# Optimization experiments

Measured on AMD Instinct MI355X. Metric: run time of the kernel, lower is better.

Reference implementation:

```python
import math
import jax, jax.numpy as jnp
import numpy as np

N, M = 2048, 128            # fine grid points, coarse points
IN_NF, H, LMAX = 256, 128, 2
A2B = 1.88973
MIN_STD = 0.32 * A2B / 2.0  # two stddevs reach min covalent radius (Bohr)
MAX_STD = 2.32 * A2B / 2.0


def _sph_lmax2(d):
    # norm-normalized real spherical harmonics (e3nn convention), unit input d[..., 3]
    x, y, z = d[..., 0], d[..., 1], d[..., 2]
    s3 = math.sqrt(3.0)
    sh0 = jnp.ones_like(x)[..., None]                                    # [., 1]
    sh1 = jnp.stack([x, y, z], axis=-1)                                  # [., 3]
    sh2 = jnp.stack([s3 * x * z, s3 * x * y,
                     y * y - 0.5 * (x * x + z * z),
                     s3 * y * z, 0.5 * s3 * (z * z - x * x)], axis=-1)   # [., 5]
    return [sh0, sh1, sh2]


def _radial(dist, nb):
    # Gaussian radial basis; two stddevs span [MIN_COV_RAD, MAX_COV_RAD]
    s = jnp.linspace(MIN_STD, MAX_STD, nb, dtype=dist.dtype)
    temps = 2.0 * s * s
    x2 = dist[..., None] ** 2
    return jnp.exp(-x2 / temps) * (2.0 / 3.0) * x2 / temps / (math.pi * temps) ** 1.5


def setup_inputs():
    key = jax.random.key(0)
    k = jax.random.split(key, 10)
    xav = math.sqrt(6.0 / (H + H))
    return {
        'h': jax.random.normal(k[0], (N, IN_NF), jnp.float32),
        'grid_coords': jax.random.normal(k[1], (N, 3), jnp.float32),
        'coarse_coords': jax.random.normal(k[2], (M, 3), jnp.float32),
        'grid_weights': jax.random.uniform(k[3], (N,), jnp.float32),
        'W_pre': jax.random.normal(k[4], (IN_NF, H), jnp.float32) * math.sqrt(2.0 / (IN_NF + H)),
        'b_pre': jnp.zeros((H,), jnp.float32),
        'W_down': jax.random.uniform(k[5], (LMAX + 1, H, H), jnp.float32, -xav, xav),
        'W_up': jax.random.uniform(k[6], (LMAX + 1, H, H), jnp.float32, -xav, xav),
        'W_post': jax.random.normal(k[7], (H, H), jnp.float32) * math.sqrt(2.0 / (H + H)),
        'b_post': jnp.zeros((H,), jnp.float32),
    }


def reference(h, grid_coords, coarse_coords, grid_weights,
              W_pre, b_pre, W_down, W_up, W_post, b_post):
    h = jax.nn.silu(h @ W_pre + b_pre)                            # [N, H]
    # all-pairs directions/distances (vect_cdist); radius_cutoff = inf -> every pair is an edge
    dvec = grid_coords[:, None, :] - coarse_coords[None, :, :]    # [N, M, 3]
    dist = jnp.sqrt((dvec * dvec + 1e-20).sum(-1))                # [N, M]
    dirs = dvec / dist[..., None]
    sh = _sph_lmax2(dirs)                                         # list of [N, M, 2l+1]
    rad = _radial(dist, H)                                        # [N, M, H]
    # tp_down: paths (0e x le -> le); l=0 uses the scalar branch (no 1/sqrt(2l+1))
    # radial gating per hidden channel + quadrature integration onto coarse nodes
    coarse = []
    for l in range(LMAX + 1):
        norm = 1.0 if l == 0 else math.sqrt(2 * l + 1)
        c = jnp.einsum('nu,uw,nmj,nmw,n->mwj',
                       h, W_down[l], sh[l], rad, grid_weights) / norm
        coarse.append(c)                                          # [M, H, 2l+1]
    # tp_up: paths (le x le -> 0e); l>0 branch divides by sqrt(2l+1); scatter back to grid
    out = 0.0
    for l in range(LMAX + 1):
        norm = 1.0 if l == 0 else math.sqrt(2 * l + 1)
        out = out + jnp.einsum('mui,uw,nmi->nw', coarse[l], W_up[l], sh[l]) / norm
    return jax.nn.silu(out @ W_post + b_post)                     # [N, H]
```

## Files before the change

kernel.cpp:

```cpp
#include <hip/hip_runtime.h>
#include <math.h>

#define N_PTS 2048
#define M_PTS 128
#define INNF  256
#define H     128

#define MIN_STDC 0.30235680f
#define MAX_STDC 2.19208680f
#define PI_F     3.14159265358979f
#define LOG2E_F  1.44269504089f

static __device__ __forceinline__ float silu_f(float x) {
  return x / (1.0f + __expf(-x));
}

__global__ __launch_bounds__(256) void k_pre(const float* __restrict__ h,
    const float* __restrict__ W_pre, const float* __restrict__ b_pre,
    const float* __restrict__ W_down, const float* __restrict__ gw,
    float* __restrict__ hdg4) {
  __shared__ float h_lds[4 * INNF];
  __shared__ float hp_lds[4 * H];
  __shared__ float red[4 * 3 * H];
  int t = threadIdx.x;
  int n0 = blockIdx.x * 4;
  int lw  = t & 31;
  int row = (t >> 5) & 3;
  int uh  = t >> 7;
  int w0 = lw * 4;
  int n  = n0 + row;

  {
    int r4 = t >> 6, c4i = (t & 63) << 2;
    *(float4*)&h_lds[r4 * INNF + c4i] =
        *(const float4*)(h + (size_t)(n0 + r4) * INNF + c4i);
  }
  __syncthreads();

  float a1[4] = {};
  for (int u = uh * 128; u < uh * 128 + 128; u += 2) {
    float hv0 = h_lds[row * INNF + u];
    float hv1 = h_lds[row * INNF + u + 1];
    float4 wv0 = *(const float4*)(W_pre + (size_t)u * H + w0);
    float4 wv1 = *(const float4*)(W_pre + (size_t)(u + 1) * H + w0);
    a1[0] += hv0 * wv0.x + hv1 * wv1.x;
    a1[1] += hv0 * wv0.y + hv1 * wv1.y;
    a1[2] += hv0 * wv0.z + hv1 * wv1.z;
    a1[3] += hv0 * wv0.w + hv1 * wv1.w;
  }
  if (uh == 1) {
    #pragma unroll
    for (int i = 0; i < 4; ++i) red[row * H + w0 + i] = a1[i];
  }
  __syncthreads();
  if (uh == 0) {
    float4 bv = *(const float4*)(b_pre + w0);
    float bb[4] = {bv.x, bv.y, bv.z, bv.w};
    #pragma unroll
    for (int i = 0; i < 4; ++i)
      hp_lds[row * H + w0 + i] = silu_f(a1[i] + red[row * H + w0 + i] + bb[i]);
  }
  __syncthreads();

  float a2[3][4] = {};
  for (int u = uh * 64; u < uh * 64 + 64; ++u) {
    float p = hp_lds[row * H + u];
    #pragma unroll
    for (int l = 0; l < 3; ++l) {
      float4 wv = *(const float4*)(W_down + ((size_t)l * H + u) * H + w0);
      a2[l][0] += p * wv.x; a2[l][1] += p * wv.y;
      a2[l][2] += p * wv.z; a2[l][3] += p * wv.w;
    }
  }
  if (uh == 1) {
    #pragma unroll
    for (int l = 0; l < 3; ++l)
      #pragma unroll
      for (int i = 0; i < 4; ++i)
        red[(row * 3 + l) * H + w0 + i] = a2[l][i];
  }
  __syncthreads();
  if (uh == 0) {
    const float stp = (MAX_STDC - MIN_STDC) / 127.0f;
    const float invn1 = 0.57735026919f, invn2 = 0.44721359550f;
    float gwv = gw[n];
    #pragma unroll
    for (int i = 0; i < 4; ++i) {
      int w = w0 + i;
      float s = MIN_STDC + (float)w * stp;
      float temps = 2.0f * s * s;
      float coef = (2.0f / 3.0f) / (temps * powf(PI_F * temps, 1.5f));
      float sc = gwv * coef;
      float v0 = (a2[0][i] + red[(row * 3 + 0) * H + w]) * sc;
      float v1 = (a2[1][i] + red[(row * 3 + 1) * H + w]) * sc * invn1;
      float v2 = (a2[2][i] + red[(row * 3 + 2) * H + w]) * sc * invn2;
      *(float4*)(hdg4 + ((size_t)n * H + w) * 4) = make_float4(v0, v1, v2, 0.0f);
    }
  }
}

__global__ __launch_bounds__(256) void k_down(const float* __restrict__ gc,
    const float* __restrict__ cc, const float* __restrict__ hdg4,
    float* __restrict__ c_part) {
  __shared__ float lds[4608];
  int t = threadIdx.x;
  int m0 = blockIdx.x * 4;
  int ss = blockIdx.y;
  int n0 = ss * 64;
  int w  = t & 127;
  int nh = t >> 7;

  {
    int n_loc = t >> 2, m_loc = t & 3;
    int n = n0 + n_loc, m = m0 + m_loc;
    float dx = gc[3*n]   - cc[3*m];
    float dy = gc[3*n+1] - cc[3*m+1];
    float dz = gc[3*n+2] - cc[3*m+2];
    float d2 = dx*dx + dy*dy + dz*dz + 3e-20f;
    float inv = rsqrtf(d2);
    float x = dx*inv, y = dy*inv, z = dz*inv;
    const float s3 = 1.73205080757f;
    float* dst = &lds[(size_t)t * 12];
    dst[0] = 1.0f; dst[1] = x; dst[2] = y; dst[3] = z;
    dst[4] = s3*x*z; dst[5] = s3*x*y; dst[6] = y*y - 0.5f*(x*x + z*z);
    dst[7] = s3*y*z; dst[8] = 0.5f*s3*(z*z - x*x);
    dst[9] = d2; dst[10] = 0.0f; dst[11] = 0.0f;
  }
  __syncthreads();

  const float stp = (MAX_STDC - MIN_STDC) / 127.0f;
  float sw = MIN_STDC + (float)w * stp;
  float m_nl2t = -LOG2E_F / (2.0f * sw * sw);

  float acc[4][9] = {};
  for (int j = 0; j < 32; j += 4) {
    float4 hv[4];
    #pragma unroll
    for (int q = 0; q < 4; ++q)
      hv[q] = *(const float4*)(hdg4 + ((size_t)(n0 + nh*32 + j + q)*H + w)*4);
    #pragma unroll
    for (int q = 0; q < 4; ++q) {
      const float* shb = &lds[(size_t)(nh*32 + j + q) * 48];
      #pragma unroll
      for (int mm = 0; mm < 4; ++mm) {
        float4 q0 = *(const float4*)(shb + mm*12);
        float4 q1 = *(const float4*)(shb + mm*12 + 4);
        float4 q2 = *(const float4*)(shb + mm*12 + 8);
        float e  = exp2f(q2.y * m_nl2t);
        float rp = e * q2.y;
        float t0 = hv[q].x*rp, t1 = hv[q].y*rp, t2 = hv[q].z*rp;
        acc[mm][0] += t0;
        acc[mm][1] += t1*q0.y; acc[mm][2] += t1*q0.z; acc[mm][3] += t1*q0.w;
        acc[mm][4] += t2*q1.x; acc[mm][5] += t2*q1.y;
        acc[mm][6] += t2*q1.z; acc[mm][7] += t2*q1.w;
        acc[mm][8] += t2*q2.x;
      }
    }
  }

  __syncthreads();
  if (nh == 1) {
    #pragma unroll
    for (int mm = 0; mm < 4; ++mm)
      #pragma unroll
      for (int li = 0; li < 9; ++li)
        lds[(mm*9 + li)*128 + w] = acc[mm][li];
  }
  __syncthreads();
  if (nh == 0) {
    #pragma unroll
    for (int mm = 0; mm < 4; ++mm)
      #pragma unroll
      for (int li = 0; li < 9; ++li) {
        float v = acc[mm][li] + lds[(mm*9 + li)*128 + w];
        c_part[(((size_t)ss*M_PTS + m0 + mm)*9 + li)*H + w] = v;
      }
  }
}

__global__ __launch_bounds__(128) void k_cu(const float* __restrict__ c_part,
    const float* __restrict__ W_up, float* __restrict__ CU9) {
  __shared__ float c_lds[H];
  int t = threadIdx.x;
  int m = blockIdx.x, li = blockIdx.y;
  float v = 0.0f;
  #pragma unroll 8
  for (int s = 0; s < 32; ++s)
    v += c_part[(((size_t)s*M_PTS + m)*9 + li)*H + t];
  c_lds[t] = v;
  __syncthreads();

  int l = (li == 0) ? 0 : (li < 4 ? 1 : 2);
  const float invn[3] = {1.0f, 0.57735026919f, 0.44721359550f};
  float acc = 0.0f;
  for (int u = 0; u < H; u += 4) {
    float w0 = W_up[((size_t)l*H + u + 0)*H + t];
    float w1 = W_up[((size_t)l*H + u + 1)*H + t];
    float w2 = W_up[((size_t)l*H + u + 2)*H + t];
    float w3 = W_up[((size_t)l*H + u + 3)*H + t];
    acc += c_lds[u]*w0 + c_lds[u+1]*w1 + c_lds[u+2]*w2 + c_lds[u+3]*w3;
  }
  CU9[((size_t)m*9 + li)*H + t] = acc * invn[l];
}

__global__ __launch_bounds__(256) void k_up(const float* __restrict__ gc,
    const float* __restrict__ cc, const float* __restrict__ CU9,
    float* __restrict__ out_part) {
  __shared__ float At[72 * 36];
  __shared__ float Bl[72 * 128];
  int t = threadIdx.x;
  int n0 = blockIdx.x * 32;
  int ks = blockIdx.y;
  int wq  = t & 31;
  int tgn = t >> 5;
  int w0 = wq * 4;

  {
    int ch = t >> 7, idx = t & 127;
    int n_loc = idx >> 2, m_loc = idx & 3;
    int mrel = ch*4 + m_loc;
    int n = n0 + n_loc, m = ks*8 + mrel;
    float dx = gc[3*n]   - cc[3*m];
    float dy = gc[3*n+1] - cc[3*m+1];
    float dz = gc[3*n+2] - cc[3*m+2];
    float d2 = dx*dx + dy*dy + dz*dz + 3e-20f;
    float inv = rsqrtf(d2);
    float x = dx*inv, y = dy*inv, z = dz*inv;
    const float s3 = 1.73205080757f;
    float sh[9];
    sh[0] = 1.0f; sh[1] = x; sh[2] = y; sh[3] = z;
    sh[4] = s3*x*z; sh[5] = s3*x*y; sh[6] = y*y - 0.5f*(x*x + z*z);
    sh[7] = s3*y*z; sh[8] = 0.5f*s3*(z*z - x*x);
    #pragma unroll
    for (int li = 0; li < 9; ++li)
      At[(mrel*9 + li)*36 + n_loc] = sh[li];
  }
  #pragma unroll
  for (int i = 0; i < 9; ++i) {
    int idx = t + i*256;
    *(float4*)&Bl[idx*4] = *(const float4*)(CU9 + (size_t)ks*72*H + idx*4);
  }
  __syncthreads();

  float acc[4][4] = {};
  #pragma unroll 8
  for (int k = 0; k < 72; ++k) {
    float4 a = *(const float4*)&At[k*36 + 4*tgn];
    float4 b = *(const float4*)&Bl[k*128 + w0];
    float av[4] = {a.x, a.y, a.z, a.w};
    float bv[4] = {b.x, b.y, b.z, b.w};
    #pragma unroll
    for (int r = 0; r < 4; ++r)
      #pragma unroll
      for (int c = 0; c < 4; ++c)
        acc[r][c] += av[r] * bv[c];
  }
  #pragma unroll
  for (int r = 0; r < 4; ++r) {
    size_t row = (size_t)ks*N_PTS + n0 + 4*tgn + r;
    *(float4*)(out_part + row*H + w0) =
        make_float4(acc[r][0], acc[r][1], acc[r][2], acc[r][3]);
  }
}

__global__ __launch_bounds__(256) void k_post(const float* __restrict__ out_part,
    const float* __restrict__ W_post, const float* __restrict__ b_post,
    float* __restrict__ out) {
  __shared__ float op[4 * H];
  int t = threadIdx.x;
  int n0 = blockIdx.x * 4;
  int w = t & 127, nh = t >> 7;

  #pragma unroll
  for (int i = 0; i < 2; ++i) {
    int idx = t + i*256;
    int nl = idx >> 7, ww = idx & 127;
    float v = 0.0f;
    #pragma unroll
    for (int s = 0; s < 16; ++s)
      v += out_part[((size_t)s*N_PTS + n0 + nl)*H + ww];
    op[nl*H + ww] = v;
  }
  __syncthreads();

  float acc[2] = {0.0f, 0.0f};
  for (int u = 0; u < H; u += 4) {
    float4 p0 = *(const float4*)&op[(nh*2 + 0)*H + u];
    float4 p1 = *(const float4*)&op[(nh*2 + 1)*H + u];
    float w0 = W_post[(u+0)*H + w];
    float w1 = W_post[(u+1)*H + w];
    float w2 = W_post[(u+2)*H + w];
    float w3 = W_post[(u+3)*H + w];
    acc[0] += p0.x*w0 + p0.y*w1 + p0.z*w2 + p0.w*w3;
    acc[1] += p1.x*w0 + p1.y*w1 + p1.z*w2 + p1.w*w3;
  }
  float bp = b_post[w];
  out[(size_t)(n0 + nh*2 + 0)*H + w] = silu_f(acc[0] + bp);
  out[(size_t)(n0 + nh*2 + 1)*H + w] = silu_f(acc[1] + bp);
}

extern "C" void kernel_launch(void* const* d_in, const int* in_sizes, int n_in,
                              void* d_out, int out_size, void* d_ws, size_t ws_size,
                              hipStream_t stream) {
  const float* h      = (const float*)d_in[0];
  const float* gc     = (const float*)d_in[1];
  const float* cc     = (const float*)d_in[2];
  const float* gw     = (const float*)d_in[3];
  const float* W_pre  = (const float*)d_in[4];
  const float* b_pre  = (const float*)d_in[5];
  const float* W_down = (const float*)d_in[6];
  const float* W_up   = (const float*)d_in[7];
  const float* W_post = (const float*)d_in[8];
  const float* b_post = (const float*)d_in[9];

  float* ws       = (float*)d_ws;
  float* hdg4     = ws;
  float* c_part   = hdg4 + 1048576;
  float* CU9      = c_part + 4718592;
  float* out_part = c_part;
  float* out      = (float*)d_out;

  k_pre <<<512,           256, 0, stream>>>(h, W_pre, b_pre, W_down, gw, hdg4);
  k_down<<<dim3(32,32),   256, 0, stream>>>(gc, cc, hdg4, c_part);
  k_cu  <<<dim3(128,9),   128, 0, stream>>>(c_part, W_up, CU9);
  k_up  <<<dim3(64,16),   256, 0, stream>>>(gc, cc, CU9, out_part);
  k_post<<<512,           256, 0, stream>>>(out_part, W_post, b_post, out);
}
```

Before: 155.7 us.

## Stage W_pre and W_down tiles in LDS and process 8 rows per block

The pre-projection kernel now handles 8 grid points per block, with each of the 8 warps owning one row. Chunks of W_pre and W_down are cooperatively staged into shared memory and reused across all 8 rows. The old split-K across two half-blocks, with its shared-memory reduction, is removed, and the grid is halved. This targets redundant global weight reads at the cost of more synchronisation and a larger LDS footprint (about 60KB), which may limit occupancy. Only the first of five kernels changes, so the effect on total time is bounded.

```diff
diff --git a/kernel.cpp b/kernel.cpp
--- a/kernel.cpp
+++ b/kernel.cpp
@@ -19,70 +19,84 @@
     const float* __restrict__ W_pre, const float* __restrict__ b_pre,
     const float* __restrict__ W_down, const float* __restrict__ gw,
     float* __restrict__ hdg4) {
-  __shared__ float h_lds[4 * INNF];
-  __shared__ float hp_lds[4 * H];
-  __shared__ float red[4 * 3 * H];
-  int t = threadIdx.x;
-  int n0 = blockIdx.x * 4;
-  int lw  = t & 31;
-  int row = (t >> 5) & 3;
-  int uh  = t >> 7;
+  __shared__ float bigW[12288];
+  __shared__ float h_t[8 * INNF];
+  __shared__ float hp_t[8 * H];
+  int t = threadIdx.x;
+  int n0 = blockIdx.x * 8;
+  int lw = t & 31;
+  int g  = t >> 5;
   int w0 = lw * 4;
-  int n  = n0 + row;
-
+
+  #pragma unroll
+  for (int i = 0; i < 2; ++i) {
+    int idx = t + i * 256;
+    int row = idx >> 6, col = (idx & 63) << 2;
+    *(float4*)&h_t[row * INNF + col] =
+        *(const float4*)(h + (size_t)(n0 + row) * INNF + col);
+  }
+
+  float acc[4] = {};
+  for (int kc = 0; kc < 256; kc += 64) {
+    __syncthreads();
+    #pragma unroll
+    for (int i = 0; i < 8; ++i) {
+      int idx = t + i * 256;
+      *(float4*)&bigW[idx * 4] = *(const float4*)(W_pre + (size_t)kc * H + idx * 4);
+    }
+    __syncthreads();
+    #pragma unroll 4
+    for (int u4 = 0; u4 < 16; ++u4) {
+      float4 hv = *(const float4*)&h_t[g * INNF + kc + u4 * 4];
+      float hvv[4] = {hv.x, hv.y, hv.z, hv.w};
+      #pragma unroll
+      for (int uu = 0; uu < 4; ++uu) {
+        float4 wv = *(const float4*)&bigW[(u4 * 4 + uu) * H + w0];
+        acc[0] += hvv[uu] * wv.x; acc[1] += hvv[uu] * wv.y;
+        acc[2] += hvv[uu] * wv.z; acc[3] += hvv[uu] * wv.w;
+      }
+    }
+  }
   {
-    int r4 = t >> 6, c4i = (t & 63) << 2;
-    *(float4*)&h_lds[r4 * INNF + c4i] =
-        *(const float4*)(h + (size_t)(n0 + r4) * INNF + c4i);
-  }
-  __syncthreads();
-
-  float a1[4] = {};
-  for (int u = uh * 128; u < uh * 128 + 128; u += 2) {
-    float hv0 = h_lds[row * INNF + u];
-    float hv1 = h_lds[row * INNF + u + 1];
-    float4 wv0 = *(const float4*)(W_pre + (size_t)u * H + w0);
-    float4 wv1 = *(const float4*)(W_pre + (size_t)(u + 1) * H + w0);
-    a1[0] += hv0 * wv0.x + hv1 * wv1.x;
-    a1[1] += hv0 * wv0.y + hv1 * wv1.y;
-    a1[2] += hv0 * wv0.z + hv1 * wv1.z;
-    a1[3] += hv0 * wv0.w + hv1 * wv1.w;
-  }
-  if (uh == 1) {
-    #pragma unroll
-    for (int i = 0; i < 4; ++i) red[row * H + w0 + i] = a1[i];
-  }
-  __syncthreads();
-  if (uh == 0) {
     float4 bv = *(const float4*)(b_pre + w0);
-    float bb[4] = {bv.x, bv.y, bv.z, bv.w};
-    #pragma unroll
-    for (int i = 0; i < 4; ++i)
-      hp_lds[row * H + w0 + i] = silu_f(a1[i] + red[row * H + w0 + i] + bb[i]);
-  }
-  __syncthreads();
-
-  float a2[3][4] = {};
-  for (int u = uh * 64; u < uh * 64 + 64; ++u) {
-    float p = hp_lds[row * H + u];
-    #pragma unroll
-    for (int l = 0; l < 3; ++l) {
-      float4 wv = *(const float4*)(W_down + ((size_t)l * H + u) * H + w0);
-      a2[l][0] += p * wv.x; a2[l][1] += p * wv.y;
-      a2[l][2] += p * wv.z; a2[l][3] += p * wv.w;
-    }
-  }
-  if (uh == 1) {
-    #pragma unroll
-    for (int l = 0; l < 3; ++l)
-      #pragma unroll
-      for (int i = 0; i < 4; ++i)
-        red[(row * 3 + l) * H + w0 + i] = a2[l][i];
-  }
-  __syncthreads();
-  if (uh == 0) {
+    float4 o = make_float4(silu_f(acc[0] + bv.x), silu_f(acc[1] + bv.y),
+                           silu_f(acc[2] + bv.z), silu_f(acc[3] + bv.w));
+    __syncthreads();
+    *(float4*)&hp_t[g * H + w0] = o;
+  }
+
+  float acc2[3][4] = {};
+  for (int kc = 0; kc < 128; kc += 32) {
+    __syncthreads();
+    #pragma unroll
+    for (int i = 0; i < 12; ++i) {
+      int idx = t + i * 256;
+      int l = idx >> 10, r4 = idx & 1023;
+      *(float4*)&bigW[idx * 4] =
+          *(const float4*)(W_down + ((size_t)l * H + kc) * H + r4 * 4);
+    }
+    __syncthreads();
+    #pragma unroll 2
+    for (int u4 = 0; u4 < 8; ++u4) {
+      float4 pv = *(const float4*)&hp_t[g * H + kc + u4 * 4];
+      float pvv[4] = {pv.x, pv.y, pv.z, pv.w};
+      #pragma unroll
+      for (int uu = 0; uu < 4; ++uu) {
+        int ul = u4 * 4 + uu;
+        #pragma unroll
+        for (int l = 0; l < 3; ++l) {
+          float4 wv = *(const float4*)&bigW[(l * 32 + ul) * H + w0];
+          acc2[l][0] += pvv[uu] * wv.x; acc2[l][1] += pvv[uu] * wv.y;
+          acc2[l][2] += pvv[uu] * wv.z; acc2[l][3] += pvv[uu] * wv.w;
+        }
+      }
+    }
+  }
+
+  {
     const float stp = (MAX_STDC - MIN_STDC) / 127.0f;
     const float invn1 = 0.57735026919f, invn2 = 0.44721359550f;
+    int n = n0 + g;
     float gwv = gw[n];
     #pragma unroll
     for (int i = 0; i < 4; ++i) {
@@ -91,10 +105,9 @@
       float temps = 2.0f * s * s;
       float coef = (2.0f / 3.0f) / (temps * powf(PI_F * temps, 1.5f));
       float sc = gwv * coef;
-      float v0 = (a2[0][i] + red[(row * 3 + 0) * H + w]) * sc;
-      float v1 = (a2[1][i] + red[(row * 3 + 1) * H + w]) * sc * invn1;
-      float v2 = (a2[2][i] + red[(row * 3 + 2) * H + w]) * sc * invn2;
-      *(float4*)(hdg4 + ((size_t)n * H + w) * 4) = make_float4(v0, v1, v2, 0.0f);
+      *(float4*)(hdg4 + ((size_t)n * H + w) * 4) =
+          make_float4(acc2[0][i] * sc, acc2[1][i] * sc * invn1,
+                      acc2[2][i] * sc * invn2, 0.0f);
     }
   }
 }
@@ -320,7 +333,7 @@
   float* out_part = c_part;
   float* out      = (float*)d_out;
 
-  k_pre <<<512,           256, 0, stream>>>(h, W_pre, b_pre, W_down, gw, hdg4);
+  k_pre <<<256,           256, 0, stream>>>(h, W_pre, b_pre, W_down, gw, hdg4);
   k_down<<<dim3(32,32),   256, 0, stream>>>(gc, cc, hdg4, c_part);
   k_cu  <<<dim3(128,9),   128, 0, stream>>>(c_part, W_up, CU9);
   k_up  <<<dim3(64,16),   256, 0, stream>>>(gc, cc, CU9, out_part);
```

Measured after the change: 147.3 us. -5.4%, faster.
